# Performance work log

Hardware: AMD Instinct MI355X
Metric: run time of the kernel (lower is better)

The kernel has to match this reference:

```python
import jax, jax.numpy as jnp
import numpy as np

NTOKENS = 50257
NHID = 1024
NTOK_PER_CLASS = 225   # ceil(sqrt(50257))
NCLASSES = 224         # ceil(50257/225)
BATCH = 2048


def setup_inputs() -> dict:
    key = jax.random.key(0)
    k1, k2, k3, k4 = jax.random.split(key, 4)
    initrange = 0.1
    inputs = jax.random.normal(k1, (BATCH, NHID), dtype=jnp.float32)
    labels = jax.random.randint(k2, (BATCH,), 0, NTOKENS, dtype=jnp.int64)
    layer_top_W = jax.random.uniform(k3, (NHID, NCLASSES), dtype=jnp.float32,
                                     minval=-initrange, maxval=initrange)
    layer_top_b = jnp.zeros((NCLASSES,), dtype=jnp.float32)
    layer_bottom_W = jax.random.uniform(k4, (NCLASSES, NHID, NTOK_PER_CLASS),
                                        dtype=jnp.float32,
                                        minval=-initrange, maxval=initrange)
    layer_bottom_b = jnp.zeros((NCLASSES, NTOK_PER_CLASS), dtype=jnp.float32)
    return {"inputs": inputs, "labels": labels,
            "layer_top_W": layer_top_W, "layer_top_b": layer_top_b,
            "layer_bottom_W": layer_bottom_W, "layer_bottom_b": layer_bottom_b}


def reference(inputs, labels, layer_top_W, layer_top_b, layer_bottom_W, layer_bottom_b):
    batch_size = inputs.shape[0]
    label_position_top = labels // NTOK_PER_CLASS          # [B]
    label_position_bottom = labels % NTOK_PER_CLASS        # [B]

    # top-level class probabilities
    top_logits = inputs @ layer_top_W + layer_top_b        # [B, nclasses]
    top_probs = jax.nn.softmax(top_logits, axis=1)

    # per-sample gather of class weight matrices + batched matmul
    W_sel = layer_bottom_W[label_position_top]             # [B, nhid, ntok_per_class]
    b_sel = layer_bottom_b[label_position_top]             # [B, ntok_per_class]
    bottom_logits = jnp.einsum('bh,bht->bt', inputs, W_sel) + b_sel
    bottom_probs = jax.nn.softmax(bottom_logits, axis=1)

    idx = jnp.arange(batch_size)
    target_probs = top_probs[idx, label_position_top] * bottom_probs[idx, label_position_bottom]
    return target_probs
```

## Files before the change

kernel.cpp:

```cpp
#include <hip/hip_runtime.h>
#include <math.h>

#define NHID  1024
#define NCLS  224
#define NTPC  225
#define BATCH 2048

#define NBOT_BLOCKS (NCLS * 4)
#define NTOP_BLOCKS (128 * 4)

#define CLS_OFF  0
#define POS_OFF  8192
#define LIST_OFF 16384
#define OFFS_OFF 24576
#define YTOP_OFF 32768
#define YTOP_BYTES (BATCH * NCLS * 4)
#define YBOT_OFF (YTOP_OFF + YTOP_BYTES)
#define YBOT_BYTES (BATCH * NTPC * 4)

__global__ __launch_bounds__(256) void group_kernel(const int* __restrict__ labels,
                                                    int* __restrict__ cls,
                                                    int* __restrict__ pos,
                                                    int* __restrict__ list,
                                                    int* __restrict__ offs) {
    __shared__ int cnt[NCLS];
    __shared__ int sc[256];
    __shared__ int bex[NCLS];
    __shared__ int nz;
    const int tid = threadIdx.x;
    if (tid == 0) nz = 0;
    for (int j = tid; j < NCLS; j += 256) cnt[j] = 0;
    __syncthreads();
    int loc = 0;
    for (int k = 0; k < 4; ++k) {
        int i = tid + 256 * k;
        if (labels[2 * i + 1] != 0) loc = 1;
    }
    if (loc) atomicOr(&nz, 1);
    __syncthreads();
    const bool is64 = (nz == 0);
    int myc[8], myr[8];
#pragma unroll
    for (int k = 0; k < 8; ++k) {
        int i = tid + 256 * k;
        int l = is64 ? labels[2 * i] : labels[i];
        int c = l / NTPC;
        cls[i] = c;
        pos[i] = l - c * NTPC;
        myc[k] = c;
        myr[k] = atomicAdd(&cnt[c], 1);
    }
    __syncthreads();
    int v = (tid < NCLS) ? cnt[tid] : 0;
    sc[tid] = v;
    __syncthreads();
    for (int off = 1; off < 256; off <<= 1) {
        int u = (tid >= off) ? sc[tid - off] : 0;
        __syncthreads();
        sc[tid] += u;
        __syncthreads();
    }
    if (tid < NCLS) {
        int ex = sc[tid] - v;
        bex[tid] = ex;
        offs[tid] = ex;
    }
    if (tid == 0) offs[NCLS] = BATCH;
    __syncthreads();
#pragma unroll
    for (int k = 0; k < 8; ++k) {
        int i = tid + 256 * k;
        list[bex[myc[k]] + myr[k]] = i;
    }
}

__global__ __launch_bounds__(256) void partial_kernel(const float* __restrict__ x,
                                                      const float* __restrict__ Wt,
                                                      const float* __restrict__ Wb,
                                                      const int* __restrict__ list,
                                                      const int* __restrict__ offs,
                                                      float* __restrict__ ytop,
                                                      float* __restrict__ ybot) {
    __shared__ __align__(16) float xs[256 * 16];
    const int tid = threadIdx.x;
    const int w = tid >> 6, l = tid & 63;
    const int bi = blockIdx.x;
    const bool isBot = (bi < NBOT_BLOCKS);

    int k, o, n, ycols;
    const float* W;
    float* y;
    if (isBot) {
        int c = bi >> 2; k = bi & 3;
        o = offs[c]; n = offs[c + 1] - o;
        W = Wb + (size_t)c * (NHID * NTPC);
        y = ybot; ycols = NTPC;
    } else {
        int b2 = bi - NBOT_BLOCKS;
        int st = b2 >> 2; k = b2 & 3;
        o = st * 16; n = 16;
        W = Wt; y = ytop; ycols = NCLS;
    }
    const int hbase = k * 256;
    const int col   = 64 * w + l;
    const int colc  = min(col, ycols - 1);
    const bool colok = (col < ycols);
    const int hq = (tid >> 1) & 3;

    for (int tile = 0; tile * 16 < n; ++tile) {
        if (tile) __syncthreads();
        const float* xcol = x + hbase + tid;
#pragma unroll
        for (int i = 0; i < 16; ++i) {
            int idx = tile * 16 + i;
            int s = isBot ? list[o + min(idx, n - 1)] : (o + i);
            xs[(tid << 4) + ((((i >> 2) ^ hq) << 2) | (i & 3))] = xcol[(size_t)s * NHID];
        }
        __syncthreads();

        float acc[16];
#pragma unroll
        for (int i = 0; i < 16; ++i) acc[i] = 0.f;

        const float* wr = W + (size_t)hbase * ycols + colc;
#pragma unroll 8
        for (int h = 0; h < 256; ++h) {
            float wv = wr[0];
            const float4* xr = (const float4*)&xs[h << 4];
            const int q = (h >> 1) & 3;
            float4 x0 = xr[q];
            float4 x1 = xr[1 ^ q];
            float4 x2 = xr[2 ^ q];
            float4 x3 = xr[3 ^ q];
            acc[0]  = fmaf(x0.x, wv, acc[0]);
            acc[1]  = fmaf(x0.y, wv, acc[1]);
            acc[2]  = fmaf(x0.z, wv, acc[2]);
            acc[3]  = fmaf(x0.w, wv, acc[3]);
            acc[4]  = fmaf(x1.x, wv, acc[4]);
            acc[5]  = fmaf(x1.y, wv, acc[5]);
            acc[6]  = fmaf(x1.z, wv, acc[6]);
            acc[7]  = fmaf(x1.w, wv, acc[7]);
            acc[8]  = fmaf(x2.x, wv, acc[8]);
            acc[9]  = fmaf(x2.y, wv, acc[9]);
            acc[10] = fmaf(x2.z, wv, acc[10]);
            acc[11] = fmaf(x2.w, wv, acc[11]);
            acc[12] = fmaf(x3.x, wv, acc[12]);
            acc[13] = fmaf(x3.y, wv, acc[13]);
            acc[14] = fmaf(x3.z, wv, acc[14]);
            acc[15] = fmaf(x3.w, wv, acc[15]);
            wr += ycols;
        }

        const int nt = min(n - tile * 16, 16);
        if (colok) {
            for (int i = 0; i < nt; ++i) {
                int s = isBot ? list[o + tile * 16 + i] : (o + i);
                atomicAdd(&y[(size_t)s * ycols + col], acc[i]);
            }
        }
    }
}

__global__ __launch_bounds__(256) void finalize_kernel(const float* __restrict__ ytop,
                                                       const float* __restrict__ ybot,
                                                       const float* __restrict__ bt,
                                                       const float* __restrict__ bb,
                                                       const int* __restrict__ cls,
                                                       const int* __restrict__ pos,
                                                       float* __restrict__ out) {
    const int w = threadIdx.x >> 6, l = threadIdx.x & 63;
    const int s = blockIdx.x * 4 + w;
    const int c = cls[s], p = pos[s];

    float v[4];
#pragma unroll
    for (int g = 0; g < 4; ++g) {
        int col = l + 64 * g;
        v[g] = (col < NCLS) ? ytop[(size_t)s * NCLS + col] + bt[col] : -INFINITY;
    }
    float mx = fmaxf(fmaxf(v[0], v[1]), fmaxf(v[2], v[3]));
#pragma unroll
    for (int off = 32; off; off >>= 1) mx = fmaxf(mx, __shfl_xor(mx, off));
    float sum = 0.f, tc = 0.f;
#pragma unroll
    for (int g = 0; g < 4; ++g) {
        int col = l + 64 * g;
        float e = (col < NCLS) ? __expf(v[g] - mx) : 0.f;
        sum += e;
        if (col == c) tc = e;
    }
#pragma unroll
    for (int off = 32; off; off >>= 1) {
        sum += __shfl_xor(sum, off);
        tc  += __shfl_xor(tc, off);
    }
    const float tp = tc / sum;

#pragma unroll
    for (int g = 0; g < 4; ++g) {
        int col = l + 64 * g;
        v[g] = (col < NTPC) ? ybot[(size_t)s * NTPC + col] + bb[c * NTPC + col] : -INFINITY;
    }
    mx = fmaxf(fmaxf(v[0], v[1]), fmaxf(v[2], v[3]));
#pragma unroll
    for (int off = 32; off; off >>= 1) mx = fmaxf(mx, __shfl_xor(mx, off));
    float bsum = 0.f, ep = 0.f;
#pragma unroll
    for (int g = 0; g < 4; ++g) {
        int col = l + 64 * g;
        float e = (col < NTPC) ? __expf(v[g] - mx) : 0.f;
        bsum += e;
        if (col == p) ep = e;
    }
#pragma unroll
    for (int off = 32; off; off >>= 1) bsum += __shfl_xor(bsum, off);
    int owner = ((l == (p & 63)) && ((p >> 6) == ((l + 64 * ((p >> 6))) == p ? (p >> 6) : -1)));
#pragma unroll
    for (int g = 0; g < 4; ++g)
        if (l + 64 * g == p) out[s] = tp * ep / bsum;
    (void)owner;
}

extern "C" void kernel_launch(void* const* d_in, const int* in_sizes, int n_in,
                              void* d_out, int out_size, void* d_ws, size_t ws_size,
                              hipStream_t stream) {
    const float* inputs = (const float*)d_in[0];
    const int*   labels = (const int*)d_in[1];
    const float* topW   = (const float*)d_in[2];
    const float* topB   = (const float*)d_in[3];
    const float* botW   = (const float*)d_in[4];
    const float* botB   = (const float*)d_in[5];
    float* out = (float*)d_out;

    char* ws   = (char*)d_ws;
    int*   cls = (int*)(ws + CLS_OFF);
    int*   pos = (int*)(ws + POS_OFF);
    int*   lst = (int*)(ws + LIST_OFF);
    int*   off = (int*)(ws + OFFS_OFF);
    float* ytop = (float*)(ws + YTOP_OFF);
    float* ybot = (float*)(ws + YBOT_OFF);

    hipMemsetAsync(ws + YTOP_OFF, 0, YTOP_BYTES + YBOT_BYTES, stream);
    group_kernel<<<1, 256, 0, stream>>>(labels, cls, pos, lst, off);
    partial_kernel<<<NBOT_BLOCKS + NTOP_BLOCKS, 256, 0, stream>>>(
        inputs, topW, botW, lst, off, ytop, ybot);
    finalize_kernel<<<BATCH / 4, 256, 0, stream>>>(ytop, ybot, topB, botB, cls, pos, out);
}
```

Baseline: 344.1 us.

## Split hidden dimension eight ways and template partial kernel per branch

Raises the K-split of the partial GEMM from 4 to 8 chunks of 128 hidden units, doubling the block count to improve GPU occupancy and load balance on the skewed per-class groups. Specializes the bottom and top paths through a templated helper with compile-time column counts, reorders block indexing so k-splits are the outer dimension, and adds a launch-bounds occupancy hint. The shared x tile is halved and loaded cooperatively by two thread halves. It doubles the number of atomic adds into the output accumulators and re-reads x rows more often.

```diff
diff --git a/kernel.cpp b/kernel.cpp
--- a/kernel.cpp
+++ b/kernel.cpp
@@ -6,8 +6,11 @@
 #define NTPC  225
 #define BATCH 2048
 
-#define NBOT_BLOCKS (NCLS * 4)
-#define NTOP_BLOCKS (128 * 4)
+#define KSPLIT 8
+#define KCH    128
+#define NTILES (BATCH / 16)
+#define NBOT_BLOCKS (NCLS * KSPLIT)
+#define NTOP_BLOCKS (NTILES * KSPLIT)
 
 #define CLS_OFF  0
 #define POS_OFF  8192
@@ -74,47 +77,31 @@
     }
 }
 
-__global__ __launch_bounds__(256) void partial_kernel(const float* __restrict__ x,
-                                                      const float* __restrict__ Wt,
-                                                      const float* __restrict__ Wb,
-                                                      const int* __restrict__ list,
-                                                      const int* __restrict__ offs,
-                                                      float* __restrict__ ytop,
-                                                      float* __restrict__ ybot) {
-    __shared__ __align__(16) float xs[256 * 16];
+template<int YC, bool BOT>
+__device__ __forceinline__ void run_tiles(const float* __restrict__ x,
+                                          const float* __restrict__ W,
+                                          float* __restrict__ y,
+                                          const int* __restrict__ list,
+                                          int o, int n, int hbase,
+                                          float* __restrict__ xs) {
     const int tid = threadIdx.x;
     const int w = tid >> 6, l = tid & 63;
-    const int bi = blockIdx.x;
-    const bool isBot = (bi < NBOT_BLOCKS);
-
-    int k, o, n, ycols;
-    const float* W;
-    float* y;
-    if (isBot) {
-        int c = bi >> 2; k = bi & 3;
-        o = offs[c]; n = offs[c + 1] - o;
-        W = Wb + (size_t)c * (NHID * NTPC);
-        y = ybot; ycols = NTPC;
-    } else {
-        int b2 = bi - NBOT_BLOCKS;
-        int st = b2 >> 2; k = b2 & 3;
-        o = st * 16; n = 16;
-        W = Wt; y = ytop; ycols = NCLS;
-    }
-    const int hbase = k * 256;
-    const int col   = 64 * w + l;
-    const int colc  = min(col, ycols - 1);
-    const bool colok = (col < ycols);
-    const int hq = (tid >> 1) & 3;
+    const int col  = 64 * w + l;
+    const int colc = min(col, YC - 1);
+    const bool colok = (col < YC);
+    const int r  = tid & 127;
+    const int hs = tid >> 7;
+    const int rq = (r >> 1) & 3;
 
     for (int tile = 0; tile * 16 < n; ++tile) {
         if (tile) __syncthreads();
-        const float* xcol = x + hbase + tid;
-#pragma unroll
-        for (int i = 0; i < 16; ++i) {
-            int idx = tile * 16 + i;
-            int s = isBot ? list[o + min(idx, n - 1)] : (o + i);
-            xs[(tid << 4) + ((((i >> 2) ^ hq) << 2) | (i & 3))] = xcol[(size_t)s * NHID];
+        const float* xrow = x + hbase + r;
+#pragma unroll
+        for (int j = 0; j < 8; ++j) {
+            const int i = hs * 8 + j;
+            const int idx = tile * 16 + i;
+            const int s = BOT ? list[o + min(idx, n - 1)] : (o + idx);
+            xs[(r << 4) + ((((i >> 2) ^ rq) << 2) | (i & 3))] = xrow[(size_t)s * NHID];
         }
         __syncthreads();
 
@@ -122,9 +109,9 @@
 #pragma unroll
         for (int i = 0; i < 16; ++i) acc[i] = 0.f;
 
-        const float* wr = W + (size_t)hbase * ycols + colc;
+        const float* wr = W + (size_t)hbase * YC + colc;
 #pragma unroll 8
-        for (int h = 0; h < 256; ++h) {
+        for (int h = 0; h < KCH; ++h) {
             float wv = wr[0];
             const float4* xr = (const float4*)&xs[h << 4];
             const int q = (h >> 1) & 3;
@@ -148,16 +135,40 @@
             acc[13] = fmaf(x3.y, wv, acc[13]);
             acc[14] = fmaf(x3.z, wv, acc[14]);
             acc[15] = fmaf(x3.w, wv, acc[15]);
-            wr += ycols;
+            wr += YC;
         }
 
         const int nt = min(n - tile * 16, 16);
         if (colok) {
             for (int i = 0; i < nt; ++i) {
-                int s = isBot ? list[o + tile * 16 + i] : (o + i);
-                atomicAdd(&y[(size_t)s * ycols + col], acc[i]);
+                const int s = BOT ? list[o + tile * 16 + i] : (o + tile * 16 + i);
+                atomicAdd(&y[(size_t)s * YC + col], acc[i]);
             }
         }
+    }
+}
+
+__global__ __launch_bounds__(256, 8) void partial_kernel(const float* __restrict__ x,
+                                                         const float* __restrict__ Wt,
+                                                         const float* __restrict__ Wb,
+                                                         const int* __restrict__ list,
+                                                         const int* __restrict__ offs,
+                                                         float* __restrict__ ytop,
+                                                         float* __restrict__ ybot) {
+    __shared__ __align__(16) float xs[KCH * 16];
+    const int bi = blockIdx.x;
+    if (bi < NBOT_BLOCKS) {
+        const int c = bi % NCLS;
+        const int k = bi / NCLS;
+        const int o = offs[c];
+        const int n = offs[c + 1] - o;
+        run_tiles<NTPC, true>(x, Wb + (size_t)c * (NHID * NTPC), ybot, list,
+                              o, n, k * KCH, xs);
+    } else {
+        const int b2 = bi - NBOT_BLOCKS;
+        const int st = b2 % NTILES;
+        const int k  = b2 / NTILES;
+        run_tiles<NCLS, false>(x, Wt, ytop, list, st * 16, 16, k * KCH, xs);
     }
 }
 
@@ -214,11 +225,9 @@
     }
 #pragma unroll
     for (int off = 32; off; off >>= 1) bsum += __shfl_xor(bsum, off);
-    int owner = ((l == (p & 63)) && ((p >> 6) == ((l + 64 * ((p >> 6))) == p ? (p >> 6) : -1)));
 #pragma unroll
     for (int g = 0; g < 4; ++g)
         if (l + 64 * g == p) out[s] = tp * ep / bsum;
-    (void)owner;
 }
 
 extern "C" void kernel_launch(void* const* d_in, const int* in_sizes, int n_in,
```

New measurement: 355.4 us. 1.03x slower.
